# Performance work log

Measured on AMD Instinct MI355X. Metric: run time of the kernel, lower is better.

## Reference

```python
import jax, jax.numpy as jnp
import numpy as np

# task -> non-background class ids, padded with -1 to fixed width 3
NBG = np.array([[0, 1, 2], [0, 3, 4], [0, 5, 6], [0, 7, 8],
                [0, 9, -1], [0, 10, -1], [0, 11, -1]], dtype=np.int32)
NEG = -1e9      # pad logit (finite stand-in for -inf, grad-safe)
SMOOTH = 1e-5
NUM_CLASSES = 12


def setup_inputs() -> dict:
    key = jax.random.key(0)
    k1, k2, k3 = jax.random.split(key, 3)
    B, C, D, H, W = 4, 12, 32, 128, 128
    inputs = jax.random.normal(k1, (B, C, D, H, W), dtype=jnp.float32)
    task_id = jax.random.randint(k2, (B,), 0, 7, dtype=jnp.int32)
    # build targets consistent with each sample's task: labels in task_nbg[task]
    raw = jax.random.randint(k3, (B, D, H, W), 0, 3, dtype=jnp.int32)
    nbg = jnp.asarray(NBG)
    ids = nbg[task_id]                                   # [B,3]
    valid_max = jnp.where(ids[:, 2] < 0, 1, 2)           # 2-class tasks: raw in {0,1}
    raw = jnp.minimum(raw, valid_max[:, None, None, None])
    targets = jnp.take_along_axis(ids, raw.reshape(B, -1), axis=1).reshape(B, D, H, W)
    return {"inputs": inputs, "targets": targets, "task_id": task_id}


def reference(inputs, targets, task_id):
    B = inputs.shape[0]
    probs = jax.nn.softmax(inputs, axis=1)               # [B,12,D,H,W]
    nbg = jnp.asarray(NBG)
    ids = nbg[task_id]                                   # [B,3]
    mask = (ids >= 0)                                    # [B,3]
    idsc = jnp.maximum(ids, 0)
    mask5 = mask[:, :, None, None, None]
    gathered = jnp.take_along_axis(probs, idsc[:, :, None, None, None], axis=1)  # [B,3,D,H,W]
    score = jnp.where(mask5, gathered, 0.0)

    # --- remapped marginal targets: labels > 0 shifted by delta ---
    t = task_id.astype(jnp.int32)
    delta = jnp.where(t <= 4, -2 * t, -t - 4)
    tm = jnp.where(targets > 0, targets + delta[:, None, None, None], targets)   # in {0,1,2}

    # --- marginal CE: log_softmax over gathered probs (note: probs, not logits, matching torch F.cross_entropy on softmaxed inputs) ---
    logits = jnp.where(mask5, gathered, NEG)
    logp = jax.nn.log_softmax(logits, axis=1)
    nll = -jnp.take_along_axis(logp, tm[:, None], axis=1)[:, 0]                  # [B,D,H,W]
    loss_marg_ce = nll.mean(axis=(1, 2, 3)).sum() / B

    # --- marginal dice (padded classes contribute exactly 0) ---
    tgt = ((targets[:, None] == idsc[:, :, None, None, None]) & mask5).astype(probs.dtype)
    inter = jnp.sum(score * tgt, axis=(2, 3, 4))
    y_sum = jnp.sum(tgt, axis=(2, 3, 4))                 # tgt is binary: tgt*tgt == tgt
    z_sum = jnp.sum(score * score, axis=(2, 3, 4))
    dice = (2 * inter + SMOOTH) / (z_sum + y_sum + SMOOTH)
    loss_marg_dice = (1.0 - dice).sum() / B

    # --- exclusion: target_e = 1 - onehot(targets, 0..11), class 0 zeroed ---
    cls = jnp.arange(NUM_CLASSES, dtype=targets.dtype)[None, :, None, None, None]
    onehot = (targets[:, None] == cls).astype(probs.dtype)
    te = 1.0 - onehot
    te = te.at[:, 0].set(0.0)
    inter_e = jnp.sum(probs * te, axis=(2, 3, 4))
    y_e = jnp.sum(te, axis=(2, 3, 4))
    z_e = jnp.sum(probs * probs, axis=(2, 3, 4))
    dice_e = (2 * inter_e + SMOOTH) / (z_e + y_e + SMOOTH)
    loss_exc_dice = dice_e.sum() / B                     # inv=True: sum of dice scores

    loss_exc_ce = (jnp.log1p(probs) * te).mean(axis=(2, 3, 4)).sum() / B

    return (loss_marg_dice, loss_marg_ce, loss_exc_dice, loss_exc_ce)
```

## Files before the change

kernel.cpp:

```cpp
#include <hip/hip_runtime.h>


#define S2 262144
#define BLOCKS_PER_B 256
#define THREADS 256
#define ITERS 4
#define NVOX 524288.0f
#define SMOOTH 1e-5f

#define WRED(v) { v += __shfl_down(v,32); v += __shfl_down(v,16); \
                  v += __shfl_down(v,8);  v += __shfl_down(v,4);  \
                  v += __shfl_down(v,2);  v += __shfl_down(v,1); }

#define PROC2(COMP) do {                                                       \
  float xv[12];                                                                \
  _Pragma("unroll")                                                            \
  for (int c = 0; c < 12; ++c) xv[c] = x[c].COMP;                              \
  const int tgt = tg.COMP;                                                     \
  float m = xv[0];                                                             \
  _Pragma("unroll")                                                            \
  for (int c = 1; c < 12; ++c) m = fmaxf(m, xv[c]);                            \
  float e[12]; float es = 0.f;                                                 \
  _Pragma("unroll")                                                            \
  for (int c = 0; c < 12; ++c) { e[c] = __expf(xv[c] - m); es += e[c]; }       \
  const float r = __builtin_amdgcn_rcpf(es);                                   \
  float p[12];                                                                 \
  _Pragma("unroll")                                                            \
  for (int c = 0; c < 12; ++c) {                                               \
    p[c] = e[c] * r;                                                           \
    aZ[c] += p[c] * p[c];                                                      \
    aP[c] += p[c];                                                             \
  }                                                                            \
    \
  float q = 1.f;                                                               \
  _Pragma("unroll")                                                            \
  for (int c = 1; c < 12; ++c) q = __builtin_fmaf(p[c], q, q);                 \
  const float g0 = p[0];                                                       \
  float g1 = 0.f, g2 = 0.f;                                                    \
  _Pragma("unroll")                                                            \
  for (int c = 1; c < 12; ++c) {                                               \
    if (c==1||c==3||c==5||c==7||c==9||c==10||c==11) g1 = (id1==c) ? p[c] : g1; \
    else                                            g2 = (id2==c) ? p[c] : g2; \
  }                                                                            \
  const bool t0 = (tgt == 0);                                                  \
  const bool t1 = (tgt == id1);                                                \
  const bool t2 = (tgt == id2);              \
  c0 += t0 ? 1.f : 0.f;  c1 += t1 ? 1.f : 0.f;  c2 += t2 ? 1.f : 0.f;          \
  p0S += t0 ? g0 : 0.f;  p1S += t1 ? g1 : 0.f;  p2S += t2 ? g2 : 0.f;          \
  const float pt = t1 ? g1 : (t2 ? g2 : 0.f);                                  \
  cesE += __logf(q * __builtin_amdgcn_rcpf(1.f + pt));                         \
       \
  float s3 = __expf(g0) + __expf(g1);                                          \
  if (v2) s3 += __expf(g2);                                                    \
  const float gt = t0 ? g0 : (t1 ? g1 : g2);                                   \
  ces += __logf(s3) - gt;                                                      \
} while (0)

__global__ void zero_acc(float* __restrict__ acc) {
  acc[threadIdx.x] = 0.f;
}

__global__ __launch_bounds__(THREADS, 4)
void marg_main(const float2* __restrict__ inp, const int2* __restrict__ tgtp,
               const int* __restrict__ task_id, float* __restrict__ acc) {
  const int b   = blockIdx.x / BLOCKS_PER_B;
  const int blk = blockIdx.x % BLOCKS_PER_B;
  const int t   = task_id[b];
  const int id1 = (t <= 4) ? 2*t + 1 : t + 5;
  const int id2 = (t <= 3) ? 2*t + 2 : -1;
  const bool v2 = (id2 >= 0);

  const float2* inB = inp  + (size_t)b * 12 * S2;
  const int2*   tgB = tgtp + (size_t)b * S2;

  float aZ[12], aP[12];
  #pragma unroll
  for (int c = 0; c < 12; ++c) { aZ[c]=0.f; aP[c]=0.f; }
  float ces=0.f, cesE=0.f, c0=0.f, c1=0.f, c2=0.f, p0S=0.f, p1S=0.f, p2S=0.f;

  #pragma unroll 1
  for (int it = 0; it < ITERS; ++it) {
    const int s = (blk * ITERS + it) * THREADS + (int)threadIdx.x;
    float2 x[12];
    #pragma unroll
    for (int c = 0; c < 12; ++c) x[c] = inB[c * S2 + s];
    const int2 tg = tgB[s];
    PROC2(x); PROC2(y);
  }

  WRED(ces); WRED(cesE); WRED(c0); WRED(c1); WRED(c2);
  WRED(p0S); WRED(p1S); WRED(p2S);
  #pragma unroll
  for (int c = 0; c < 12; ++c) { WRED(aZ[c]); WRED(aP[c]); }

  __shared__ float red[4][32];
  const int lane = threadIdx.x & 63;
  const int wv   = threadIdx.x >> 6;
  if (lane == 0) {
    float* rw = red[wv];
    rw[0]=ces; rw[1]=cesE; rw[2]=c0; rw[3]=c1; rw[4]=c2;
    rw[5]=p0S; rw[6]=p1S; rw[7]=p2S;
    #pragma unroll
    for (int c = 0; c < 12; ++c) { rw[8+c]=aZ[c]; rw[20+c]=aP[c]; }
  }
  __syncthreads();
  if (threadIdx.x < 32) {
    const float sv = red[0][threadIdx.x] + red[1][threadIdx.x]
                   + red[2][threadIdx.x] + red[3][threadIdx.x];
    atomicAdd(acc + b * 64 + threadIdx.x, sv);
  }
}

__global__ void finalize(const float* __restrict__ acc,
                         const int* __restrict__ task_id,
                         float* __restrict__ out) {
  if (threadIdx.x != 0) return;
  float lmd = 0.f, lmce = 0.f, led = 0.f, lece = 0.f;
  for (int b = 0; b < 4; ++b) {
    const float* a = acc + b * 64;
    const int t   = task_id[b];
    const int id1 = (t <= 4) ? 2*t + 1 : t + 5;
    const int id2 = (t <= 3) ? 2*t + 2 : -1;

    lmce += a[0] / NVOX;
    lece += a[1] / NVOX;

    const float d0 = (2.f*a[5] + SMOOTH) / (a[8 + 0]   + a[2] + SMOOTH);
    const float d1 = (2.f*a[6] + SMOOTH) / (a[8 + id1] + a[3] + SMOOTH);
    float d2 = 1.f;
    if (id2 >= 0)
      d2 = (2.f*a[7] + SMOOTH) / (a[8 + id2] + a[4] + SMOOTH);
    lmd += (1.f - d0) + (1.f - d1) + (1.f - d2);

    led += SMOOTH / (a[8] + SMOOTH);
    for (int c = 1; c < 12; ++c) {
      const float ptc  = (c == id1) ? a[6] : ((c == id2) ? a[7] : 0.f);
      const float cntc = (c == id1) ? a[3] : ((c == id2) ? a[4] : 0.f);
      const float inter = a[20 + c] - ptc;
      const float ye    = NVOX - cntc;
      led += (2.f*inter + SMOOTH) / (a[8 + c] + ye + SMOOTH);
    }
  }
  out[0] = lmd  * 0.25f;
  out[1] = lmce * 0.25f;
  out[2] = led  * 0.25f;
  out[3] = lece * 0.25f;
}

extern "C" void kernel_launch(void* const* d_in, const int* in_sizes, int n_in,
                              void* d_out, int out_size, void* d_ws, size_t ws_size,
                              hipStream_t stream) {
  const float* inputs  = (const float*)d_in[0];
  const int*   targets = (const int*)d_in[1];
  const int*   task_id = (const int*)d_in[2];
  float* out = (float*)d_out;
  float* acc = (float*)d_ws;

  zero_acc<<<1, 256, 0, stream>>>(acc);
  marg_main<<<dim3(4 * BLOCKS_PER_B), THREADS, 0, stream>>>(
      (const float2*)inputs, (const int2*)targets, task_id, acc);
  finalize<<<1, 64, 0, stream>>>(acc, task_id, out);
}
```

Before: 166.7 us.

## Double-buffer loads in main loop and replace atomics with per-block partials

The main loop is manually unrolled into two register buffers, so the loads for the next iteration are issued before the current one is processed, which hides global memory latency. The global atomicAdd accumulation is replaced by per-block partial writes that the finalize kernel reduces in parallel, and this removes the zero_acc launch. The cost is higher register pressure from the two 12-float2 buffers, which could lower occupancy under launch_bounds(256,4), and a somewhat heavier finalize kernel.

```diff
diff --git a/kernel.cpp b/kernel.cpp
--- a/kernel.cpp
+++ b/kernel.cpp
@@ -12,11 +12,11 @@
                   v += __shfl_down(v,8);  v += __shfl_down(v,4);  \
                   v += __shfl_down(v,2);  v += __shfl_down(v,1); }
 
-#define PROC2(COMP) do {                                                       \
+#define PROC2(X, TG, COMP) do {                                                \
   float xv[12];                                                                \
   _Pragma("unroll")                                                            \
-  for (int c = 0; c < 12; ++c) xv[c] = x[c].COMP;                              \
-  const int tgt = tg.COMP;                                                     \
+  for (int c = 0; c < 12; ++c) xv[c] = X[c].COMP;                              \
+  const int tgt = TG.COMP;                                                     \
   float m = xv[0];                                                             \
   _Pragma("unroll")                                                            \
   for (int c = 1; c < 12; ++c) m = fmaxf(m, xv[c]);                            \
@@ -31,7 +31,6 @@
     aZ[c] += p[c] * p[c];                                                      \
     aP[c] += p[c];                                                             \
   }                                                                            \
-    \
   float q = 1.f;                                                               \
   _Pragma("unroll")                                                            \
   for (int c = 1; c < 12; ++c) q = __builtin_fmaf(p[c], q, q);                 \
@@ -44,21 +43,25 @@
   }                                                                            \
   const bool t0 = (tgt == 0);                                                  \
   const bool t1 = (tgt == id1);                                                \
-  const bool t2 = (tgt == id2);              \
+  const bool t2 = (tgt == id2);                                                \
   c0 += t0 ? 1.f : 0.f;  c1 += t1 ? 1.f : 0.f;  c2 += t2 ? 1.f : 0.f;          \
   p0S += t0 ? g0 : 0.f;  p1S += t1 ? g1 : 0.f;  p2S += t2 ? g2 : 0.f;          \
   const float pt = t1 ? g1 : (t2 ? g2 : 0.f);                                  \
   cesE += __logf(q * __builtin_amdgcn_rcpf(1.f + pt));                         \
-       \
   float s3 = __expf(g0) + __expf(g1);                                          \
   if (v2) s3 += __expf(g2);                                                    \
   const float gt = t0 ? g0 : (t1 ? g1 : g2);                                   \
   ces += __logf(s3) - gt;                                                      \
 } while (0)
 
-__global__ void zero_acc(float* __restrict__ acc) {
-  acc[threadIdx.x] = 0.f;
-}
+#define PROCPAIR(X, T) { PROC2(X, T, x); PROC2(X, T, y); }
+
+#define LOADP(X, T, IT) do {                                                   \
+  const int s_ = sBase + (IT) * THREADS;                                       \
+  _Pragma("unroll")                                                            \
+  for (int c = 0; c < 12; ++c) X[c] = inB[c * S2 + s_];                        \
+  T = tgB[s_];                                                                 \
+} while (0)
 
 __global__ __launch_bounds__(THREADS, 4)
 void marg_main(const float2* __restrict__ inp, const int2* __restrict__ tgtp,
@@ -72,21 +75,20 @@
 
   const float2* inB = inp  + (size_t)b * 12 * S2;
   const int2*   tgB = tgtp + (size_t)b * S2;
+  const int sBase = blk * (ITERS * THREADS) + (int)threadIdx.x;
 
   float aZ[12], aP[12];
   #pragma unroll
   for (int c = 0; c < 12; ++c) { aZ[c]=0.f; aP[c]=0.f; }
   float ces=0.f, cesE=0.f, c0=0.f, c1=0.f, c2=0.f, p0S=0.f, p1S=0.f, p2S=0.f;
 
-  #pragma unroll 1
-  for (int it = 0; it < ITERS; ++it) {
-    const int s = (blk * ITERS + it) * THREADS + (int)threadIdx.x;
-    float2 x[12];
-    #pragma unroll
-    for (int c = 0; c < 12; ++c) x[c] = inB[c * S2 + s];
-    const int2 tg = tgB[s];
-    PROC2(x); PROC2(y);
-  }
+  float2 xA[12], xB[12]; int2 tA, tB;
+  LOADP(xA, tA, 0);
+  LOADP(xB, tB, 1);
+  PROCPAIR(xA, tA); LOADP(xA, tA, 2);
+  PROCPAIR(xB, tB); LOADP(xB, tB, 3);
+  PROCPAIR(xA, tA);
+  PROCPAIR(xB, tB);
 
   WRED(ces); WRED(cesE); WRED(c0); WRED(c1); WRED(c2);
   WRED(p0S); WRED(p1S); WRED(p2S);
@@ -107,17 +109,33 @@
   if (threadIdx.x < 32) {
     const float sv = red[0][threadIdx.x] + red[1][threadIdx.x]
                    + red[2][threadIdx.x] + red[3][threadIdx.x];
-    atomicAdd(acc + b * 64 + threadIdx.x, sv);
+    acc[(size_t)blockIdx.x * 32 + threadIdx.x] = sv;
   }
 }
 
 __global__ void finalize(const float* __restrict__ acc,
                          const int* __restrict__ task_id,
                          float* __restrict__ out) {
-  if (threadIdx.x != 0) return;
+  __shared__ float sm[4][32];
+  const int tid = threadIdx.x;
+  if (tid < 128) {
+    const int b = tid >> 5, k = tid & 31;
+    const float* base = acc + (size_t)(b * BLOCKS_PER_B) * 32 + k;
+    float s0=0.f, s1=0.f, s2=0.f, s3=0.f;
+    #pragma unroll 4
+    for (int blk = 0; blk < BLOCKS_PER_B; blk += 4) {
+      s0 += base[(size_t)(blk+0) * 32];
+      s1 += base[(size_t)(blk+1) * 32];
+      s2 += base[(size_t)(blk+2) * 32];
+      s3 += base[(size_t)(blk+3) * 32];
+    }
+    sm[b][k] = (s0 + s1) + (s2 + s3);
+  }
+  __syncthreads();
+  if (tid != 0) return;
   float lmd = 0.f, lmce = 0.f, led = 0.f, lece = 0.f;
   for (int b = 0; b < 4; ++b) {
-    const float* a = acc + b * 64;
+    const float* a = sm[b];
     const int t   = task_id[b];
     const int id1 = (t <= 4) ? 2*t + 1 : t + 5;
     const int id2 = (t <= 3) ? 2*t + 2 : -1;
@@ -156,8 +174,7 @@
   float* out = (float*)d_out;
   float* acc = (float*)d_ws;
 
-  zero_acc<<<1, 256, 0, stream>>>(acc);
   marg_main<<<dim3(4 * BLOCKS_PER_B), THREADS, 0, stream>>>(
       (const float2*)inputs, (const int2*)targets, task_id, acc);
-  finalize<<<1, 64, 0, stream>>>(acc, task_id, out);
+  finalize<<<1, 256, 0, stream>>>(acc, task_id, out);
 }
```

After: 174.9 us. 4.9% more time.
